# Performance work log

Measured on AMD Instinct MI355X. Metric: run time of the kernel, lower is better.

## Reference

```python
import jax, jax.numpy as jnp
import numpy as np

DIM = 512
HEADS = 8
DIM_HEAD = 64
INNER = HEADS * DIM_HEAD
CHUNK = 32
EPS = 1e-5


def _peg_conv(x, w, b):
    # x: (B, N, C); depthwise conv1d k=3 pad=1 applied on chunks of 32
    B, N, C = x.shape
    ns = -(-N // CHUNK)
    xp = jnp.pad(x, ((0, 0), (0, ns * CHUNK - N), (0, 0)))
    xp = xp.reshape(B * ns, CHUNK, C).transpose(0, 2, 1)  # (B*ns, C, 32)
    y = jax.lax.conv_general_dilated(
        xp, w, window_strides=(1,), padding=((1, 1),),
        dimension_numbers=("NCH", "OIH", "NCH"), feature_group_count=C)
    y = y + b[None, :, None]
    y = y.transpose(0, 2, 1).reshape(B, ns * CHUNK, C)[:, :N, :]
    return y


def _peg1d(x, w, b):
    p1 = _peg_conv(x, w, b)
    sx = jnp.roll(x, CHUNK // 2, axis=1)
    p2 = jnp.roll(_peg_conv(sx, w, b), -(CHUNK // 2), axis=1)
    return x + p1 + p2


def setup_inputs() -> dict:
    key = jax.random.key(0)
    ks = jax.random.split(key, 8)
    B, N, M = 2, 4096, 1024
    x = jax.random.normal(ks[0], (B, N, DIM), dtype=jnp.float32)
    mem = jax.random.normal(ks[1], (B, M, DIM), dtype=jnp.float32)
    w_qkv = jax.random.normal(ks[2], (DIM, 3 * INNER), dtype=jnp.float32) * 0.02
    w_out = jax.random.normal(ks[3], (INNER, DIM), dtype=jnp.float32) * 0.02
    b_out = jnp.zeros((DIM,), dtype=jnp.float32)
    ln_g = jnp.ones((DIM,), dtype=jnp.float32)
    ln_b = jnp.zeros((DIM,), dtype=jnp.float32)
    pk_w = jax.random.normal(ks[4], (DIM, 1, 3), dtype=jnp.float32) * 0.1
    pk_b = jnp.zeros((DIM,), dtype=jnp.float32)
    pv_w = jax.random.normal(ks[5], (DIM, 1, 3), dtype=jnp.float32) * 0.1
    pv_b = jnp.zeros((DIM,), dtype=jnp.float32)
    return {"x": x, "mem": mem, "ln_g": ln_g, "ln_b": ln_b,
            "w_qkv": w_qkv, "w_out": w_out, "b_out": b_out,
            "pk_w": pk_w, "pk_b": pk_b, "pv_w": pv_w, "pv_b": pv_b}


def reference(x, mem, ln_g, ln_b, w_qkv, w_out, b_out, pk_w, pk_b, pv_w, pv_b):
    B, N, _ = x.shape
    # LayerNorm
    mu = jnp.mean(x, axis=-1, keepdims=True)
    var = jnp.mean(jnp.square(x - mu), axis=-1, keepdims=True)
    xn = (x - mu) * jax.lax.rsqrt(var + EPS) * ln_g + ln_b
    qkv = xn @ w_qkv  # (B, N, 3*INNER)
    q, k, v = jnp.split(qkv, 3, axis=-1)
    # memory concat
    k = jnp.concatenate((k, mem), axis=1)
    v = jnp.concatenate((v, mem), axis=1)
    # PEG1D positional conv on k,v (excluding cls token at position 0)
    k = jnp.concatenate((k[:, :1, :], _peg1d(k[:, 1:, :], pk_w, pk_b)), axis=1)
    v = jnp.concatenate((v[:, :1, :], _peg1d(v[:, 1:, :], pv_w, pv_b)), axis=1)
    # split heads: b n (h d) -> b h n d
    Nk = k.shape[1]
    qh = q.reshape(B, N, HEADS, DIM_HEAD).transpose(0, 2, 1, 3)
    kh = k.reshape(B, Nk, HEADS, DIM_HEAD).transpose(0, 2, 1, 3)
    vh = v.reshape(B, Nk, HEADS, DIM_HEAD).transpose(0, 2, 1, 3)
    scale = DIM_HEAD ** -0.5
    dots = jnp.einsum("bhnd,bhmd->bhnm", qh, kh) * scale
    attn = jax.nn.softmax(dots, axis=-1)
    out = jnp.einsum("bhnm,bhmd->bhnd", attn, vh)
    out = out.transpose(0, 2, 1, 3).reshape(B, N, INNER)
    return out @ w_out + b_out
```

## Files before the change

### kernel.cpp

```cpp
#include <hip/hip_runtime.h>
#include <hip/hip_bf16.h>

typedef short short8 __attribute__((ext_vector_type(8)));
typedef __bf16 bf16x8 __attribute__((ext_vector_type(8)));
typedef float f32x4 __attribute__((ext_vector_type(4)));
typedef float f32x16 __attribute__((ext_vector_type(16)));
typedef unsigned int uint4v __attribute__((ext_vector_type(4)));

#define SEQ_N 4096
#define NKEYS 5120
#define PEG_L 5119

__device__ __forceinline__ float b2f(unsigned short s){
  union{unsigned u; float f;} v; v.u = ((unsigned)s)<<16; return v.f;
}
__device__ __forceinline__ unsigned short f2b(float f){
  unsigned u = __builtin_bit_cast(unsigned, f);
  u += 0x7fffu + ((u>>16)&1u);
  return (unsigned short)(u>>16);
}
__device__ __forceinline__ unsigned pkbf(float lo, float hi){
  return ((unsigned)f2b(hi) << 16) | (unsigned)f2b(lo);
}

__global__ void k_transpose_w(const float* __restrict__ src, unsigned short* __restrict__ dst,
                              int K, int Ncols){
  __shared__ float t[32][33];
  int tx = threadIdx.x, ty = threadIdx.y;
  int bx = blockIdx.x, by = blockIdx.y;
  #pragma unroll
  for (int i=0;i<4;i++){
    int r = by*32 + ty + 8*i, c = bx*32 + tx;
    t[ty+8*i][tx] = src[(size_t)r*Ncols + c];
  }
  __syncthreads();
  #pragma unroll
  for (int i=0;i<4;i++){
    int r = bx*32 + ty + 8*i, c = by*32 + tx;
    dst[(size_t)r*K + c] = f2b(t[tx][ty+8*i]);
  }
}

__global__ __launch_bounds__(256) void k_layernorm(const float* __restrict__ x,
    const float* __restrict__ g, const float* __restrict__ bb,
    unsigned short* __restrict__ xn){
  int w = threadIdx.x >> 6, l = threadIdx.x & 63;
  int row = blockIdx.x*4 + w;
  const float* xr = x + (size_t)row*512 + l*8;
  f32x4 a = *(const f32x4*)xr;
  f32x4 c4 = *(const f32x4*)(xr+4);
  float s = a[0]+a[1]+a[2]+a[3]+c4[0]+c4[1]+c4[2]+c4[3];
  #pragma unroll
  for (int d=1; d<64; d<<=1) s += __shfl_xor(s, d);
  float mu = s * (1.0f/512.0f);
  float vs = 0.f;
  #pragma unroll
  for (int i=0;i<4;i++){ float d0=a[i]-mu; vs += d0*d0; }
  #pragma unroll
  for (int i=0;i<4;i++){ float d0=c4[i]-mu; vs += d0*d0; }
  #pragma unroll
  for (int d=1; d<64; d<<=1) vs += __shfl_xor(vs, d);
  float rstd = rsqrtf(vs*(1.0f/512.0f) + 1e-5f);
  const float* gp = g + l*8;
  const float* bp = bb + l*8;
  unsigned short o[8];
  #pragma unroll
  for (int i=0;i<8;i++){
    float xi = (i<4)? a[i] : c4[i-4];
    o[i] = f2b((xi-mu)*rstd*gp[i] + bp[i]);
  }
  *(short8*)(xn + (size_t)row*512 + l*8) = *(short8*)o;
}

__global__ void k_memcat(const float* __restrict__ mem,
                         unsigned short* __restrict__ kf, unsigned short* __restrict__ vf){
  size_t e0 = ((size_t)blockIdx.x*256 + threadIdx.x)*8;
  f32x4 a = *(const f32x4*)(mem+e0);
  f32x4 c4 = *(const f32x4*)(mem+e0+4);
  unsigned short o[8];
  #pragma unroll
  for (int i=0;i<8;i++) o[i] = f2b((i<4)? a[i] : c4[i-4]);
  int c = (int)(e0 & 511);
  size_t row = e0 >> 9;
  size_t b = row >> 10, r = row & 1023;
  size_t dst = ((b*NKEYS) + 4096 + r)*512 + c;
  *(short8*)(kf+dst) = *(short8*)o;
  *(short8*)(vf+dst) = *(short8*)o;
}

template<int EPI>
__global__ __launch_bounds__(256) void k_gemm(const unsigned short* __restrict__ A,
    const unsigned short* __restrict__ BT, const float* __restrict__ bias,
    unsigned short* __restrict__ qb, unsigned short* __restrict__ kf,
    unsigned short* __restrict__ vf, float* __restrict__ outf){
  __shared__ unsigned short Al[64][72];
  __shared__ unsigned short Bl[64][72];
  const int tid = threadIdx.x;
  const int w = tid>>6, l = tid&63, m = l&15, hh = l>>4;
  const int m0 = blockIdx.x*64, n0 = blockIdx.y*64;
  const int srow = tid>>2, scg = tid&3;
  f32x4 acc[4];
  #pragma unroll
  for (int nt=0; nt<4; ++nt) acc[nt] = f32x4{0.f,0.f,0.f,0.f};
  const unsigned short* Ap = A + (size_t)(m0+srow)*512 + scg*8;
  const unsigned short* Bp = BT + (size_t)(n0+srow)*512 + scg*8;
  for (int kt=0; kt<8; ++kt){
    short8 a0 = *(const short8*)(Ap + kt*64);
    short8 a1 = *(const short8*)(Ap + kt*64 + 32);
    short8 b0 = *(const short8*)(Bp + kt*64);
    short8 b1 = *(const short8*)(Bp + kt*64 + 32);
    __syncthreads();
    *(short8*)&Al[srow][scg*8]      = a0;
    *(short8*)&Al[srow][32+scg*8]   = a1;
    *(short8*)&Bl[srow][scg*8]      = b0;
    *(short8*)&Bl[srow][32+scg*8]   = b1;
    __syncthreads();
    #pragma unroll
    for (int ks=0; ks<2; ++ks){
      bf16x8 af = *(const bf16x8*)&Al[w*16+m][ks*32 + hh*8];
      #pragma unroll
      for (int nt=0; nt<4; ++nt){
        bf16x8 bfv = *(const bf16x8*)&Bl[nt*16+m][ks*32 + hh*8];
        acc[nt] = __builtin_amdgcn_mfma_f32_16x16x32_bf16(af, bfv, acc[nt], 0,0,0);
      }
    }
  }
  #pragma unroll
  for (int nt=0; nt<4; ++nt){
    #pragma unroll
    for (int j=0; j<4; ++j){
      int grow = m0 + w*16 + 4*hh + j;
      int gcol = n0 + nt*16 + m;
      float v = acc[nt][j];
      if (EPI==0){
        int b = grow >> 12, n = grow & 4095;
        if (gcol < 512)       qb[(size_t)grow*512 + gcol] = f2b(v);
        else if (gcol < 1024) kf[((size_t)b*NKEYS + n)*512 + (gcol-512)]  = f2b(v);
        else                  vf[((size_t)b*NKEYS + n)*512 + (gcol-1024)] = f2b(v);
      } else {
        outf[(size_t)grow*512 + gcol] = v + bias[gcol];
      }
    }
  }
}

__global__ __launch_bounds__(256) void k_peg(const unsigned short* __restrict__ in,
    const float* __restrict__ w3, const float* __restrict__ bias,
    unsigned short* __restrict__ out){
  int idx = blockIdx.x*256 + threadIdx.x;
  int cg = idx & 63;
  int i  = (idx >> 6) % NKEYS;
  int b  = (idx >> 6) / NKEYS;
  int c0 = cg*8;
  const unsigned short* base = in + (size_t)b*NKEYS*512 + c0;
  unsigned short* op = out + ((size_t)b*NKEYS + i)*512 + c0;
  if (i == 0){ *(short8*)op = *(const short8*)base; return; }
  int j = i - 1;
  float wv0[8], wv1[8], wv2[8], bv[8], acc[8];
  #pragma unroll
  for (int k2=0;k2<8;k2++){
    wv0[k2] = w3[(c0+k2)*3 + 0];
    wv1[k2] = w3[(c0+k2)*3 + 1];
    wv2[k2] = w3[(c0+k2)*3 + 2];
    bv[k2]  = bias[c0+k2];
  }
  short8 xc = *(const short8*)(base + (size_t)i*512);
  #pragma unroll
  for (int k2=0;k2<8;k2++)
    acc[k2] = b2f((unsigned short)xc[k2]) * (1.0f + 2.0f*wv1[k2]) + 2.0f*bv[k2];
  int r = j & 31;
  int jj = j + 16; if (jj >= PEG_L) jj -= PEG_L;
  int r2 = jj & 31;
  if (r > 0){
    short8 xl = *(const short8*)(base + (size_t)j*512);
    #pragma unroll
    for (int k2=0;k2<8;k2++) acc[k2] += wv0[k2]*b2f((unsigned short)xl[k2]);
  }
  if (r < 31 && j+1 < PEG_L){
    short8 xr = *(const short8*)(base + (size_t)(j+2)*512);
    #pragma unroll
    for (int k2=0;k2<8;k2++) acc[k2] += wv2[k2]*b2f((unsigned short)xr[k2]);
  }
  if (r2 > 0){
    int p = jj - 17; if (p < 0) p += PEG_L;
    short8 xl = *(const short8*)(base + (size_t)(p+1)*512);
    #pragma unroll
    for (int k2=0;k2<8;k2++) acc[k2] += wv0[k2]*b2f((unsigned short)xl[k2]);
  }
  if (r2 < 31 && jj+1 < PEG_L){
    int p = jj - 15; if (p < 0) p += PEG_L;
    short8 xr = *(const short8*)(base + (size_t)(p+1)*512);
    #pragma unroll
    for (int k2=0;k2<8;k2++) acc[k2] += wv2[k2]*b2f((unsigned short)xr[k2]);
  }
  unsigned short o[8];
  #pragma unroll
  for (int k2=0;k2<8;k2++) o[k2] = f2b(acc[k2]);
  *(short8*)op = *(short8*)o;
}

__global__ __launch_bounds__(256) void k_vtrans(const unsigned short* __restrict__ vp,
                                                unsigned short* __restrict__ vpT){
  __shared__ unsigned short t[64][72];
  const int bh = blockIdx.y, b = bh>>3, h = bh&7;
  const int k0 = blockIdx.x*64;
  const int tid = threadIdx.x;
  #pragma unroll
  for (int it=0; it<2; ++it){
    int idx = tid + it*256;
    int key = idx>>3, dg = idx&7;
    short8 v = *(const short8*)(vp + ((size_t)b*NKEYS + k0+key)*512 + h*64 + dg*8);
    #pragma unroll
    for (int jj=0;jj<8;++jj) t[dg*8+jj][key] = (unsigned short)v[jj];
  }
  __syncthreads();
  #pragma unroll
  for (int it=0; it<2; ++it){
    int idx = tid + it*256;
    int d = idx>>3, kg = idx&7;
    short8 v = *(const short8*)&t[d][kg*8];
    *(short8*)(vpT + ((size_t)bh*64 + d)*NKEYS + k0 + kg*8) = v;
  }
}

__global__ __launch_bounds__(256) void k_attn(
    const unsigned short* __restrict__ qb,
    const unsigned short* __restrict__ kp,
    const unsigned short* __restrict__ vpT,
    unsigned short* __restrict__ ob){
  __shared__ unsigned short Kl[2][64][72];
  __shared__ unsigned short Vl[2][64][72];
  const int tid = threadIdx.x;
  const int w = tid >> 6, lid = tid & 63;
  const int lq = lid & 31, hi = lid >> 5;
  const int bh = blockIdx.y, b = bh >> 3, h = bh & 7;
  const int q = blockIdx.x*128 + w*32 + lq;

  bf16x8 qreg[4];
  {
    const unsigned short* qr = qb + (size_t)(b*SEQ_N + q)*512 + h*64 + hi*8;
    #pragma unroll
    for (int dt=0; dt<4; ++dt) qreg[dt] = *(const bf16x8*)(qr + dt*16);
  }

  f32x16 o0 = {}, o1 = {};
  float mraw = -3.0e38f, lsum = 0.f;

  const int srow = tid >> 2, sg = tid & 3;
  const unsigned short* kst = kp + (size_t)b*NKEYS*512 + h*64 + (size_t)srow*512 + sg*8;
  const unsigned short* vst = vpT + (size_t)bh*64*NKEYS + (size_t)srow*NKEYS + sg*8;

  {
    short8 a0 = *(const short8*)(kst);
    short8 a1 = *(const short8*)(kst + 32);
    short8 v0 = *(const short8*)(vst);
    short8 v1 = *(const short8*)(vst + 32);
    *(short8*)&Kl[0][srow][sg*8]    = a0;
    *(short8*)&Kl[0][srow][32+sg*8] = a1;
    *(short8*)&Vl[0][srow][sg*8]    = v0;
    *(short8*)&Vl[0][srow][32+sg*8] = v1;
  }
  __syncthreads();

  const float c2 = 0.18033688011f;
  int cur = 0;
  for (int kt=0; kt<80; ++kt){
    short8 a0, a1, v0s, v1s;
    const bool pf = (kt+1) < 80;
    if (pf){
      const unsigned short* kn = kst + (size_t)(kt+1)*64*512;
      const unsigned short* vn = vst + (size_t)(kt+1)*64;
      a0  = *(const short8*)(kn);
      a1  = *(const short8*)(kn + 32);
      v0s = *(const short8*)(vn);
      v1s = *(const short8*)(vn + 32);
    }

    f32x16 s0 = {}, s1 = {};
    #pragma unroll
    for (int dt=0; dt<4; ++dt){
      bf16x8 kf0 = *(const bf16x8*)&Kl[cur][lq][dt*16 + hi*8];
      s0 = __builtin_amdgcn_mfma_f32_32x32x16_bf16(kf0, qreg[dt], s0, 0,0,0);
    }
    #pragma unroll
    for (int dt=0; dt<4; ++dt){
      bf16x8 kf1 = *(const bf16x8*)&Kl[cur][32+lq][dt*16 + hi*8];
      s1 = __builtin_amdgcn_mfma_f32_32x32x16_bf16(kf1, qreg[dt], s1, 0,0,0);
    }

    float t8[8];
    #pragma unroll
    for (int i=0;i<8;++i) t8[i] = fmaxf(fmaxf(s0[i], s0[i+8]), fmaxf(s1[i], s1[i+8]));
    #pragma unroll
    for (int i=0;i<4;++i) t8[i] = fmaxf(t8[i], t8[i+4]);
    float pm = fmaxf(fmaxf(t8[0],t8[1]), fmaxf(t8[2],t8[3]));
    pm = fmaxf(pm, __shfl_xor(pm, 32, 64));

    if (!__all(pm <= mraw + 64.0f)){
      float mnew = fmaxf(mraw, pm);
      float al = exp2f((mraw - mnew)*c2);
      #pragma unroll
      for (int i=0;i<16;++i){ o0[i]*=al; o1[i]*=al; }
      lsum *= al;
      mraw = mnew;
    }
    const float mc = mraw * c2;
    #pragma unroll
    for (int i=0;i<16;++i){
      s0[i] = exp2f(fmaf(s0[i], c2, -mc));
      s1[i] = exp2f(fmaf(s1[i], c2, -mc));
    }
    float u8[8];
    #pragma unroll
    for (int i=0;i<8;++i) u8[i] = (s0[i]+s0[i+8]) + (s1[i]+s1[i+8]);
    #pragma unroll
    for (int i=0;i<4;++i) u8[i] += u8[i+4];
    float ps = (u8[0]+u8[1]) + (u8[2]+u8[3]);
    ps += __shfl_xor(ps, 32, 64);
    lsum += ps;

    float p[32];
    #pragma unroll
    for (int i=0;i<16;++i){ p[i] = s0[i]; p[16+i] = s1[i]; }
    #pragma unroll
    for (int sl=0; sl<4; ++sl){
      const int rb = sl*8;
      unsigned w0 = pkbf(p[rb+0], p[rb+1]);
      unsigned w1 = pkbf(p[rb+2], p[rb+3]);
      unsigned w2 = pkbf(p[rb+4], p[rb+5]);
      unsigned w3 = pkbf(p[rb+6], p[rb+7]);
      unsigned u0 = hi ? w0 : w2;
      unsigned u1 = hi ? w1 : w3;
      unsigned su0 = __shfl_xor(u0, 32, 64);
      unsigned su1 = __shfl_xor(u1, 32, 64);
      unsigned e0 = hi ? su0 : w0;
      unsigned e1 = hi ? su1 : w1;
      unsigned e2 = hi ? w2 : su0;
      unsigned e3 = hi ? w3 : su1;
      uint4v wv = {e0, e1, e2, e3};
      bf16x8 pb = __builtin_bit_cast(bf16x8, wv);
      bf16x8 vf0 = *(const bf16x8*)&Vl[cur][lq][sl*16 + hi*8];
      o0 = __builtin_amdgcn_mfma_f32_32x32x16_bf16(vf0, pb, o0, 0,0,0);
      bf16x8 vf1 = *(const bf16x8*)&Vl[cur][32+lq][sl*16 + hi*8];
      o1 = __builtin_amdgcn_mfma_f32_32x32x16_bf16(vf1, pb, o1, 0,0,0);
    }

    if (pf){
      *(short8*)&Kl[cur^1][srow][sg*8]    = a0;
      *(short8*)&Kl[cur^1][srow][32+sg*8] = a1;
      *(short8*)&Vl[cur^1][srow][sg*8]    = v0s;
      *(short8*)&Vl[cur^1][srow][32+sg*8] = v1s;
    }
    __syncthreads();
    cur ^= 1;
  }

  const float inv = 1.0f / lsum;
  unsigned short* obase = ob + (size_t)(b*SEQ_N + q)*512 + h*64;
  #pragma unroll
  for (int r=0; r<16; r+=2){
    const int dloc = (r&3) + 8*(r>>2) + 4*hi;
    *(unsigned*)(obase + dloc)      = pkbf(o0[r]*inv, o0[r+1]*inv);
    *(unsigned*)(obase + 32 + dloc) = pkbf(o1[r]*inv, o1[r+1]*inv);
  }
}

extern "C" void kernel_launch(void* const* d_in, const int* in_sizes, int n_in,
                              void* d_out, int out_size, void* d_ws, size_t ws_size,
                              hipStream_t stream){
  const float* x     = (const float*)d_in[0];
  const float* mem   = (const float*)d_in[1];
  const float* ln_g  = (const float*)d_in[2];
  const float* ln_b  = (const float*)d_in[3];
  const float* w_qkv = (const float*)d_in[4];
  const float* w_out = (const float*)d_in[5];
  const float* b_out = (const float*)d_in[6];
  const float* pk_w  = (const float*)d_in[7];
  const float* pk_b  = (const float*)d_in[8];
  const float* pv_w  = (const float*)d_in[9];
  const float* pv_b  = (const float*)d_in[10];
  float* outp = (float*)d_out;

  char* ws = (char*)d_ws;
  size_t off = 0;
  auto alloc = [&](size_t bytes)->void*{
    void* p = ws + off; off += (bytes + 255) & ~(size_t)255; return p;
  };
  unsigned short* wqkvT = (unsigned short*)alloc((size_t)1536*512*2);
  unsigned short* woutT = (unsigned short*)alloc((size_t)512*512*2);
  unsigned short* xn    = (unsigned short*)alloc((size_t)8192*512*2);
  unsigned short* q_b   = (unsigned short*)alloc((size_t)8192*512*2);
  unsigned short* kf    = (unsigned short*)alloc((size_t)2*NKEYS*512*2);
  unsigned short* vf    = (unsigned short*)alloc((size_t)2*NKEYS*512*2);
  unsigned short* kpg   = (unsigned short*)alloc((size_t)2*NKEYS*512*2);
  unsigned short* vpg   = (unsigned short*)alloc((size_t)2*NKEYS*512*2);
  unsigned short* vpT   = (unsigned short*)alloc((size_t)2*NKEYS*512*2);
  unsigned short* attnb = (unsigned short*)alloc((size_t)8192*512*2);

  k_transpose_w<<<dim3(48,16), dim3(32,8), 0, stream>>>(w_qkv, wqkvT, 512, 1536);
  k_transpose_w<<<dim3(16,16), dim3(32,8), 0, stream>>>(w_out, woutT, 512, 512);
  k_layernorm<<<2048, 256, 0, stream>>>(x, ln_g, ln_b, xn);
  k_memcat<<<512, 256, 0, stream>>>(mem, kf, vf);
  k_gemm<0><<<dim3(128,24), 256, 0, stream>>>(xn, wqkvT, nullptr, q_b, kf, vf, nullptr);
  k_peg<<<2560, 256, 0, stream>>>(kf, pk_w, pk_b, kpg);
  k_peg<<<2560, 256, 0, stream>>>(vf, pv_w, pv_b, vpg);
  k_vtrans<<<dim3(80,16), 256, 0, stream>>>(vpg, vpT);
  k_attn<<<dim3(32,16), 256, 0, stream>>>(q_b, kpg, vpT, attnb);
  k_gemm<1><<<dim3(128,8), 256, 0, stream>>>(attnb, woutT, b_out, nullptr, nullptr, nullptr, outp);
}
```

Measured before the change: 345.3 us.

## Split attention keys across two blocks and merge partial softmax results

Attention now splits the 5120 keys into two halves processed by separate blocks (grid z=2). Each block writes bf16 partial outputs plus the row max and sum, and a new combine kernel merges them with log-sum-exp weights. The original grid was only 512 blocks, so the split doubles parallelism to fill more CUs, at the cost of an extra kernel and extra global traffic. The change also defers the cross-half shuffle of the row sum and max, uses the hardware v_cvt_pk_bf16_f32 instruction for packing, and vectorizes the reductions. The partial buffers reuse the kf workspace region.

```diff
diff --git a/kernel.cpp b/kernel.cpp
--- a/kernel.cpp
+++ b/kernel.cpp
@@ -4,12 +4,16 @@
 typedef short short8 __attribute__((ext_vector_type(8)));
 typedef __bf16 bf16x8 __attribute__((ext_vector_type(8)));
 typedef float f32x4 __attribute__((ext_vector_type(4)));
+typedef float f32x8 __attribute__((ext_vector_type(8)));
 typedef float f32x16 __attribute__((ext_vector_type(16)));
 typedef unsigned int uint4v __attribute__((ext_vector_type(4)));
 
 #define SEQ_N 4096
 #define NKEYS 5120
 #define PEG_L 5119
+#define NSPLIT 2
+#define KEYS_PER_SPLIT 2560
+#define NT_SPLIT 40
 
 __device__ __forceinline__ float b2f(unsigned short s){
   union{unsigned u; float f;} v; v.u = ((unsigned)s)<<16; return v.f;
@@ -19,8 +23,10 @@
   u += 0x7fffu + ((u>>16)&1u);
   return (unsigned short)(u>>16);
 }
-__device__ __forceinline__ unsigned pkbf(float lo, float hi){
-  return ((unsigned)f2b(hi) << 16) | (unsigned)f2b(lo);
+__device__ __forceinline__ unsigned cvtpk(float lo, float hi){
+  unsigned r;
+  asm("v_cvt_pk_bf16_f32 %0, %1, %2" : "=v"(r) : "v"(lo), "v"(hi));
+  return r;
 }
 
 __global__ void k_transpose_w(const float* __restrict__ src, unsigned short* __restrict__ dst,
@@ -223,17 +229,19 @@
   }
 }
 
-__global__ __launch_bounds__(256) void k_attn(
+__global__ __launch_bounds__(256, 4) void k_attn(
     const unsigned short* __restrict__ qb,
     const unsigned short* __restrict__ kp,
     const unsigned short* __restrict__ vpT,
-    unsigned short* __restrict__ ob){
+    unsigned short* __restrict__ oP,
+    float* __restrict__ ml){
   __shared__ unsigned short Kl[2][64][72];
   __shared__ unsigned short Vl[2][64][72];
   const int tid = threadIdx.x;
   const int w = tid >> 6, lid = tid & 63;
   const int lq = lid & 31, hi = lid >> 5;
   const int bh = blockIdx.y, b = bh >> 3, h = bh & 7;
+  const int sp = blockIdx.z;
   const int q = blockIdx.x*128 + w*32 + lq;
 
   bf16x8 qreg[4];
@@ -247,8 +255,10 @@
   float mraw = -3.0e38f, lsum = 0.f;
 
   const int srow = tid >> 2, sg = tid & 3;
-  const unsigned short* kst = kp + (size_t)b*NKEYS*512 + h*64 + (size_t)srow*512 + sg*8;
-  const unsigned short* vst = vpT + (size_t)bh*64*NKEYS + (size_t)srow*NKEYS + sg*8;
+  const unsigned short* kst = kp + (size_t)b*NKEYS*512 + h*64
+                              + (size_t)(sp*KEYS_PER_SPLIT)*512 + (size_t)srow*512 + sg*8;
+  const unsigned short* vst = vpT + (size_t)bh*64*NKEYS + (size_t)srow*NKEYS
+                              + sp*KEYS_PER_SPLIT + sg*8;
 
   {
     short8 a0 = *(const short8*)(kst);
@@ -264,9 +274,9 @@
 
   const float c2 = 0.18033688011f;
   int cur = 0;
-  for (int kt=0; kt<80; ++kt){
+  for (int kt=0; kt<NT_SPLIT; ++kt){
     short8 a0, a1, v0s, v1s;
-    const bool pf = (kt+1) < 80;
+    const bool pf = (kt+1) < NT_SPLIT;
     if (pf){
       const unsigned short* kn = kst + (size_t)(kt+1)*64*512;
       const unsigned short* vn = vst + (size_t)(kt+1)*64;
@@ -288,47 +298,48 @@
       s1 = __builtin_amdgcn_mfma_f32_32x32x16_bf16(kf1, qreg[dt], s1, 0,0,0);
     }
 
-    float t8[8];
-    #pragma unroll
-    for (int i=0;i<8;++i) t8[i] = fmaxf(fmaxf(s0[i], s0[i+8]), fmaxf(s1[i], s1[i+8]));
-    #pragma unroll
-    for (int i=0;i<4;++i) t8[i] = fmaxf(t8[i], t8[i+4]);
-    float pm = fmaxf(fmaxf(t8[0],t8[1]), fmaxf(t8[2],t8[3]));
-    pm = fmaxf(pm, __shfl_xor(pm, 32, 64));
+    f32x8 sa0 = __builtin_shufflevector(s0, s0, 0,1,2,3,4,5,6,7);
+    f32x8 sb0 = __builtin_shufflevector(s0, s0, 8,9,10,11,12,13,14,15);
+    f32x8 sa1 = __builtin_shufflevector(s1, s1, 0,1,2,3,4,5,6,7);
+    f32x8 sb1 = __builtin_shufflevector(s1, s1, 8,9,10,11,12,13,14,15);
+    f32x8 mx8 = __builtin_elementwise_max(__builtin_elementwise_max(sa0, sb0),
+                                          __builtin_elementwise_max(sa1, sb1));
+    float pm = fmaxf(fmaxf(fmaxf(mx8[0],mx8[1]), fmaxf(mx8[2],mx8[3])),
+                     fmaxf(fmaxf(mx8[4],mx8[5]), fmaxf(mx8[6],mx8[7])));
 
     if (!__all(pm <= mraw + 64.0f)){
-      float mnew = fmaxf(mraw, pm);
+      float pg = fmaxf(pm, __shfl_xor(pm, 32, 64));
+      float mnew = fmaxf(mraw, pg);
       float al = exp2f((mraw - mnew)*c2);
       #pragma unroll
       for (int i=0;i<16;++i){ o0[i]*=al; o1[i]*=al; }
       lsum *= al;
       mraw = mnew;
     }
-    const float mc = mraw * c2;
+    const float nmc = -(mraw * c2);
     #pragma unroll
     for (int i=0;i<16;++i){
-      s0[i] = exp2f(fmaf(s0[i], c2, -mc));
-      s1[i] = exp2f(fmaf(s1[i], c2, -mc));
-    }
-    float u8[8];
-    #pragma unroll
-    for (int i=0;i<8;++i) u8[i] = (s0[i]+s0[i+8]) + (s1[i]+s1[i+8]);
-    #pragma unroll
-    for (int i=0;i<4;++i) u8[i] += u8[i+4];
-    float ps = (u8[0]+u8[1]) + (u8[2]+u8[3]);
-    ps += __shfl_xor(ps, 32, 64);
-    lsum += ps;
-
-    float p[32];
-    #pragma unroll
-    for (int i=0;i<16;++i){ p[i] = s0[i]; p[16+i] = s1[i]; }
+      s0[i] = exp2f(fmaf(s0[i], c2, nmc));
+      s1[i] = exp2f(fmaf(s1[i], c2, nmc));
+    }
+    {
+      f32x8 pa0 = __builtin_shufflevector(s0, s0, 0,1,2,3,4,5,6,7);
+      f32x8 pb0 = __builtin_shufflevector(s0, s0, 8,9,10,11,12,13,14,15);
+      f32x8 pa1 = __builtin_shufflevector(s1, s1, 0,1,2,3,4,5,6,7);
+      f32x8 pb1 = __builtin_shufflevector(s1, s1, 8,9,10,11,12,13,14,15);
+      f32x8 u = (pa0 + pb0) + (pa1 + pb1);
+      f32x4 u4 = f32x4{u[0],u[1],u[2],u[3]} + f32x4{u[4],u[5],u[6],u[7]};
+      lsum += (u4[0]+u4[1]) + (u4[2]+u4[3]);
+    }
+
     #pragma unroll
     for (int sl=0; sl<4; ++sl){
-      const int rb = sl*8;
-      unsigned w0 = pkbf(p[rb+0], p[rb+1]);
-      unsigned w1 = pkbf(p[rb+2], p[rb+3]);
-      unsigned w2 = pkbf(p[rb+4], p[rb+5]);
-      unsigned w3 = pkbf(p[rb+6], p[rb+7]);
+      const f32x16& sv = (sl < 2) ? s0 : s1;
+      const int rb = (sl & 1)*8;
+      unsigned w0 = cvtpk(sv[rb+0], sv[rb+1]);
+      unsigned w1 = cvtpk(sv[rb+2], sv[rb+3]);
+      unsigned w2 = cvtpk(sv[rb+4], sv[rb+5]);
+      unsigned w3 = cvtpk(sv[rb+6], sv[rb+7]);
       unsigned u0 = hi ? w0 : w2;
       unsigned u1 = hi ? w1 : w3;
       unsigned su0 = __shfl_xor(u0, 32, 64);
@@ -355,14 +366,45 @@
     cur ^= 1;
   }
 
-  const float inv = 1.0f / lsum;
-  unsigned short* obase = ob + (size_t)(b*SEQ_N + q)*512 + h*64;
+  const float lt = lsum + __shfl_xor(lsum, 32, 64);
+  const float inv = 1.0f / lt;
+  unsigned short* op = oP + (((size_t)(sp*16 + bh)*SEQ_N + q)*64);
   #pragma unroll
   for (int r=0; r<16; r+=2){
     const int dloc = (r&3) + 8*(r>>2) + 4*hi;
-    *(unsigned*)(obase + dloc)      = pkbf(o0[r]*inv, o0[r+1]*inv);
-    *(unsigned*)(obase + 32 + dloc) = pkbf(o1[r]*inv, o1[r+1]*inv);
-  }
+    *(unsigned*)(op + dloc)      = cvtpk(o0[r]*inv, o0[r+1]*inv);
+    *(unsigned*)(op + 32 + dloc) = cvtpk(o1[r]*inv, o1[r+1]*inv);
+  }
+  float* mlp = ml + ((size_t)(sp*16 + bh)*SEQ_N + q)*2;
+  mlp[0] = mraw;
+  mlp[1] = lt;
+}
+
+__global__ __launch_bounds__(256) void k_combine(const unsigned short* __restrict__ oP,
+    const float* __restrict__ ml, unsigned short* __restrict__ attnb){
+  const float c2 = 0.18033688011f;
+  int idx = blockIdx.x*256 + threadIdx.x;
+  int dg = idx & 7;
+  int qbh = idx >> 3;
+  int q = qbh & 4095;
+  int bh = qbh >> 12;
+  int b = bh >> 3, h = bh & 7;
+  size_t i0 = ((size_t)bh*SEQ_N + q);
+  size_t i1 = ((size_t)(16 + bh)*SEQ_N + q);
+  short8 a = *(const short8*)(oP + i0*64 + dg*8);
+  short8 c = *(const short8*)(oP + i1*64 + dg*8);
+  float m0 = ml[i0*2], l0 = ml[i0*2+1];
+  float m1 = ml[i1*2], l1 = ml[i1*2+1];
+  float ms = fmaxf(m0, m1);
+  float w0 = l0 * exp2f((m0 - ms)*c2);
+  float w1 = l1 * exp2f((m1 - ms)*c2);
+  float inv = 1.0f / (w0 + w1);
+  float a0 = w0*inv, a1 = w1*inv;
+  unsigned short o[8];
+  #pragma unroll
+  for (int k2=0;k2<8;k2++)
+    o[k2] = f2b(a0*b2f((unsigned short)a[k2]) + a1*b2f((unsigned short)c[k2]));
+  *(short8*)(attnb + ((size_t)(b*SEQ_N + q)*512) + h*64 + dg*8) = *(short8*)o;
 }
 
 extern "C" void kernel_launch(void* const* d_in, const int* in_sizes, int n_in,
@@ -397,6 +439,9 @@
   unsigned short* vpT   = (unsigned short*)alloc((size_t)2*NKEYS*512*2);
   unsigned short* attnb = (unsigned short*)alloc((size_t)8192*512*2);
 
+  unsigned short* oP = kf;
+  float* ml = (float*)((char*)kf + (size_t)NSPLIT*16*SEQ_N*64*2);
+
   k_transpose_w<<<dim3(48,16), dim3(32,8), 0, stream>>>(w_qkv, wqkvT, 512, 1536);
   k_transpose_w<<<dim3(16,16), dim3(32,8), 0, stream>>>(w_out, woutT, 512, 512);
   k_layernorm<<<2048, 256, 0, stream>>>(x, ln_g, ln_b, xn);
@@ -405,6 +450,7 @@
   k_peg<<<2560, 256, 0, stream>>>(kf, pk_w, pk_b, kpg);
   k_peg<<<2560, 256, 0, stream>>>(vf, pv_w, pv_b, vpg);
   k_vtrans<<<dim3(80,16), 256, 0, stream>>>(vpg, vpT);
-  k_attn<<<dim3(32,16), 256, 0, stream>>>(q_b, kpg, vpT, attnb);
+  k_attn<<<dim3(32,16,NSPLIT), 256, 0, stream>>>(q_b, kpg, vpT, oP, ml);
+  k_combine<<<2048, 256, 0, stream>>>(oP, ml, attnb);
   k_gemm<1><<<dim3(128,8), 256, 0, stream>>>(attnb, woutT, b_out, nullptr, nullptr, nullptr, outp);
 }
```

Result: faster. 312.7 us (-9.4%).
